# Kernel tuning notes

Measured on AMD Instinct MI355X. Metric: run time of the kernel, lower is better.

## Reference

```python
import jax, jax.numpy as jnp
import numpy as np

N, E, D = 50000, 800000, 128      # nodes, edges, input feature dim
H, HEADS, C = 128, 8, 64          # hidden units, attention heads, classes
HEAD_DIM = H // HEADS
NEG_SLOPE = 0.2


def segment_softmax(scores, seg, num_segments):
    # scores: [E, heads]; softmax over edges sharing the same destination node
    m = jax.ops.segment_max(scores, seg, num_segments=num_segments)
    ex = jnp.exp(scores - m[seg])
    s = jax.ops.segment_sum(ex, seg, num_segments=num_segments)
    return ex / (s[seg] + 1e-9)


def gcn_layer(x, src, dst, W, b):
    # mean-aggregate neighbor features along edges, then linear transform
    agg = jax.ops.segment_sum(x[src], dst, num_segments=N)          # [N, d]
    deg = jax.ops.segment_sum(jnp.ones((E,), x.dtype), dst, num_segments=N)
    agg = agg / jnp.maximum(deg, 1.0)[:, None]
    return agg @ W + b


def gat_layer(x, src, dst, Wg, a_src, a_dst, bg):
    h = (x @ Wg).reshape(N, HEADS, HEAD_DIM)                        # [N, heads, hd]
    e_s = jnp.einsum('nhd,hd->nh', h, a_src)                        # [N, heads]
    e_d = jnp.einsum('nhd,hd->nh', h, a_dst)
    scores = jax.nn.leaky_relu(e_s[src] + e_d[dst], NEG_SLOPE)      # [E, heads]
    alpha = segment_softmax(scores, dst, N)                         # [E, heads]
    msg = h[src] * alpha[:, :, None]                                # [E, heads, hd]
    out = jax.ops.segment_sum(msg, dst, num_segments=N).reshape(N, H)
    return out + bg


def setup_inputs() -> dict:
    key = jax.random.key(0)
    ks = jax.random.split(key, 12)
    s = lambda fan: 1.0 / np.sqrt(fan)
    return {
        'node_features': jax.random.normal(ks[0], (N, D), jnp.float32),
        'edge_index': jax.random.randint(ks[1], (2, E), 0, N, jnp.int32),
        'W1': jax.random.normal(ks[2], (D, H), jnp.float32) * s(D),
        'b1': jnp.zeros((H,), jnp.float32),
        'W2': jax.random.normal(ks[3], (H, H), jnp.float32) * s(H),
        'b2': jnp.zeros((H,), jnp.float32),
        'Wg': jax.random.normal(ks[4], (D, H), jnp.float32) * s(D),
        'bg': jnp.zeros((H,), jnp.float32),
        'a_src': jax.random.normal(ks[5], (HEADS, HEAD_DIM), jnp.float32) * s(HEAD_DIM),
        'a_dst': jax.random.normal(ks[6], (HEADS, HEAD_DIM), jnp.float32) * s(HEAD_DIM),
        'Wcls': jax.random.normal(ks[7], (H, C), jnp.float32) * s(H),
        'bcls': jnp.zeros((C,), jnp.float32),
        'Wl': jax.random.normal(ks[8], (H, 1), jnp.float32) * s(H),
        'bl': jnp.zeros((1,), jnp.float32),
    }


def reference(node_features, edge_index, W1, b1, W2, b2, Wg, bg, a_src, a_dst, Wcls, bcls, Wl, bl):
    src, dst = edge_index[0], edge_index[1]
    x = jax.nn.relu(gcn_layer(node_features, src, dst, W1, b1))
    x = jax.nn.relu(gcn_layer(x, src, dst, W2, b2))
    node_classification_output = jax.nn.softmax(x @ Wcls + bcls, axis=-1)  # [N, C]
    x_gat = jax.nn.relu(gat_layer(node_features, src, dst, Wg, a_src, a_dst, bg))
    link_prediction_output = jax.nn.sigmoid(x_gat @ Wl + bl)               # [N, 1]
    return (node_classification_output, link_prediction_output)
```

## Files before the change

kernel.cpp:

```cpp
#include <hip/hip_runtime.h>
#include <math.h>

#define DIM      128
#define HEADS    8
#define NCLS     64
#define NEG_SLOPE 0.2f
#define NPB32    32
#define NPB64    64
#define APAD     132
#define CAP      48

typedef unsigned int uint32;

__device__ __forceinline__ uint32 pack_bf162(float a, float b) {
    uint32 ua = __float_as_uint(a); ua += 0x7fffu + ((ua >> 16) & 1u);
    uint32 ub = __float_as_uint(b); ub += 0x7fffu + ((ub >> 16) & 1u);
    return (ua >> 16) | (ub & 0xffff0000u);
}
__device__ __forceinline__ float2 unpack_bf162(uint32 u) {
    return make_float2(__uint_as_float(u << 16), __uint_as_float(u & 0xffff0000u));
}

__global__ __launch_bounds__(256, 4)
void proj1_fill(const float* __restrict__ x, const float* __restrict__ W1,
                const float* __restrict__ Wg, const float* __restrict__ a_src,
                const float* __restrict__ a_dst, uint32* __restrict__ zb,
                float* __restrict__ e_s, float* __restrict__ e_d, int N,
                const int* __restrict__ src, const int* __restrict__ dst,
                int* __restrict__ cursor, int* __restrict__ ell, int E,
                int nProj) {
    __shared__ float A[NPB64 * APAD];
    int tid = threadIdx.x;

    if (blockIdx.x >= nProj) {
        int e = (blockIdx.x - nProj) * 256 + tid;
        if (e < E) {
            int d = dst[e];
            int pos = atomicAdd(&cursor[d], 1);
            if (pos < CAP) ell[(size_t)d * CAP + pos] = src[e];
        }
        return;
    }

    int n0 = blockIdx.x * NPB64;
    for (int idx = tid; idx < NPB64 * 32; idx += 256) {
        int nl = idx >> 5, q = idx & 31;
        int n = n0 + nl;
        float4 v = (n < N) ? ((const float4*)x)[(size_t)n * 32 + q]
                           : make_float4(0.f, 0.f, 0.f, 0.f);
        *(float4*)&A[nl * APAD + q * 4] = v;
    }
    __syncthreads();

    int fg = tid & 31, ng = tid >> 5;
    int nb = ng * 8;
    bool isG = fg >= 16;
    const float* W = isG ? (Wg + (size_t)(fg - 16) * 8) : (W1 + (size_t)fg * 8);
    float acc[8][8];
#pragma unroll
    for (int r = 0; r < 8; ++r)
#pragma unroll
        for (int c = 0; c < 8; ++c) acc[r][c] = 0.f;

#pragma unroll 4
    for (int k = 0; k < DIM; ++k) {
        float wv[8];
        *(float4*)&wv[0] = *(const float4*)(W + (size_t)k * DIM);
        *(float4*)&wv[4] = *(const float4*)(W + (size_t)k * DIM + 4);
#pragma unroll
        for (int r = 0; r < 8; ++r) {
            float a = A[(nb + r) * APAD + k];
#pragma unroll
            for (int c = 0; c < 8; ++c) acc[r][c] = fmaf(a, wv[c], acc[r][c]);
        }
    }
#pragma unroll
    for (int r = 0; r < 8; ++r) {
        int n = n0 + nb + r;
        if (n < N) {
            uint32 o[4];
#pragma unroll
            for (int c = 0; c < 4; ++c) o[c] = pack_bf162(acc[r][2 * c], acc[r][2 * c + 1]);
            *(uint4*)(zb + (size_t)n * 128 + fg * 4) = *(uint4*)o;
        }
    }
    if (isG) {
        int head = (fg - 16) >> 1, sub = ((fg - 16) & 1) * 8;
        float as[8], ad[8];
#pragma unroll
        for (int j = 0; j < 8; ++j) {
            as[j] = a_src[head * 16 + sub + j];
            ad[j] = a_dst[head * 16 + sub + j];
        }
#pragma unroll
        for (int r = 0; r < 8; ++r) {
            int n = n0 + nb + r;
            float ps = 0.f, pd = 0.f;
#pragma unroll
            for (int c = 0; c < 8; ++c) {
                ps = fmaf(acc[r][c], as[c], ps);
                pd = fmaf(acc[r][c], ad[c], pd);
            }
            ps += __shfl_xor(ps, 1);
            pd += __shfl_xor(pd, 1);
            if (n < N && !(fg & 1)) {
                e_s[n * HEADS + head] = ps;
                e_d[n * HEADS + head] = pd;
            }
        }
    }
}

__global__ __launch_bounds__(256, 8)
void mega1(const uint32* __restrict__ zb, const int* __restrict__ cursor,
           const int* __restrict__ ell, const float* __restrict__ e_s,
           const float* __restrict__ e_d, const float* __restrict__ b1,
           const float* __restrict__ bg, const float* __restrict__ Wl,
           const float* __restrict__ bl, uint32* __restrict__ x1b,
           float* __restrict__ out_link, int N) {
    int wave = threadIdx.x >> 6, lane = threadIdx.x & 63;
    int n = blockIdx.x * 4 + wave;
    if (n >= N) return;
    int eoff = lane >> 5, q = lane & 31;
    bool isH = q >= 16;
    int head = (max(q, 16) - 16) >> 1;
    float edl = e_d[n * HEADS + head];
    const uint4* zrow = (const uint4*)zb;
    size_t base = (size_t)n * CAP;
    int len = min(cursor[n], CAP);
    float acc[8];
#pragma unroll
    for (int j = 0; j < 8; ++j) acc[j] = 0.f;
    float den = 0.f;
    int it = 0;
    for (; it + 8 <= len; it += 8) {
        int s[4];
#pragma unroll
        for (int k = 0; k < 4; ++k) s[k] = ell[base + it + 2 * k + eoff];
        float es[4]; uint4 u[4];
#pragma unroll
        for (int k = 0; k < 4; ++k) {
            es[k] = e_s[s[k] * HEADS + head];
            u[k]  = zrow[(size_t)s[k] * 32 + q];
        }
#pragma unroll
        for (int k = 0; k < 4; ++k) {
            float sc = es[k] + edl;
            sc = (sc > 0.f) ? sc : NEG_SLOPE * sc;
            float ex = __expf(sc);
            den += ex;
            float w = isH ? ex : 1.f;
            float2 v0 = unpack_bf162(u[k].x), v1 = unpack_bf162(u[k].y);
            float2 v2 = unpack_bf162(u[k].z), v3 = unpack_bf162(u[k].w);
            acc[0] = fmaf(v0.x, w, acc[0]); acc[1] = fmaf(v0.y, w, acc[1]);
            acc[2] = fmaf(v1.x, w, acc[2]); acc[3] = fmaf(v1.y, w, acc[3]);
            acc[4] = fmaf(v2.x, w, acc[4]); acc[5] = fmaf(v2.y, w, acc[5]);
            acc[6] = fmaf(v3.x, w, acc[6]); acc[7] = fmaf(v3.y, w, acc[7]);
        }
    }
    for (; it < len; it += 2) {
        int e = it + eoff;
        bool valid = e < len;
        int s = ell[base + (valid ? e : it)];
        float sc = e_s[s * HEADS + head] + edl;
        sc = (sc > 0.f) ? sc : NEG_SLOPE * sc;
        float ex = __expf(sc);
        uint4 u = zrow[(size_t)s * 32 + q];
        den += valid ? ex : 0.f;
        float w = valid ? (isH ? ex : 1.f) : 0.f;
        float2 v0 = unpack_bf162(u.x), v1 = unpack_bf162(u.y);
        float2 v2 = unpack_bf162(u.z), v3 = unpack_bf162(u.w);
        acc[0] = fmaf(v0.x, w, acc[0]); acc[1] = fmaf(v0.y, w, acc[1]);
        acc[2] = fmaf(v1.x, w, acc[2]); acc[3] = fmaf(v1.y, w, acc[3]);
        acc[4] = fmaf(v2.x, w, acc[4]); acc[5] = fmaf(v2.y, w, acc[5]);
        acc[6] = fmaf(v3.x, w, acc[6]); acc[7] = fmaf(v3.y, w, acc[7]);
    }
#pragma unroll
    for (int j = 0; j < 8; ++j) acc[j] += __shfl_xor(acc[j], 32);
    den += __shfl_xor(den, 32);

    if (!isH && eoff == 0) {
        float inv = 1.f / fmaxf((float)len, 1.f);
        float4 ba = ((const float4*)b1)[2 * q];
        float4 bb = ((const float4*)b1)[2 * q + 1];
        uint4 o;
        o.x = pack_bf162(fmaxf(acc[0] * inv + ba.x, 0.f), fmaxf(acc[1] * inv + ba.y, 0.f));
        o.y = pack_bf162(fmaxf(acc[2] * inv + ba.z, 0.f), fmaxf(acc[3] * inv + ba.w, 0.f));
        o.z = pack_bf162(fmaxf(acc[4] * inv + bb.x, 0.f), fmaxf(acc[5] * inv + bb.y, 0.f));
        o.w = pack_bf162(fmaxf(acc[6] * inv + bb.z, 0.f), fmaxf(acc[7] * inv + bb.w, 0.f));
        ((uint4*)(x1b + (size_t)n * 64))[q] = o;
    }
    float p = 0.f;
    if (isH && eoff == 0) {
        float inva = 1.f / (den + 1e-9f);
        int hq = q - 16;
        float4 ga = ((const float4*)bg)[2 * hq];
        float4 gb = ((const float4*)bg)[2 * hq + 1];
        float4 wa = ((const float4*)Wl)[2 * hq];
        float4 wb = ((const float4*)Wl)[2 * hq + 1];
        p = fmaf(fmaxf(acc[0] * inva + ga.x, 0.f), wa.x, p);
        p = fmaf(fmaxf(acc[1] * inva + ga.y, 0.f), wa.y, p);
        p = fmaf(fmaxf(acc[2] * inva + ga.z, 0.f), wa.z, p);
        p = fmaf(fmaxf(acc[3] * inva + ga.w, 0.f), wa.w, p);
        p = fmaf(fmaxf(acc[4] * inva + gb.x, 0.f), wb.x, p);
        p = fmaf(fmaxf(acc[5] * inva + gb.y, 0.f), wb.y, p);
        p = fmaf(fmaxf(acc[6] * inva + gb.z, 0.f), wb.z, p);
        p = fmaf(fmaxf(acc[7] * inva + gb.w, 0.f), wb.w, p);
    }
#pragma unroll
    for (int off = 1; off < 64; off <<= 1) p += __shfl_xor(p, off);
    if (lane == 0) out_link[n] = 1.f / (1.f + expf(-(p + bl[0])));
}

__global__ __launch_bounds__(256, 4)
void proj2(const uint32* __restrict__ x1b, const float* __restrict__ W2,
           uint32* __restrict__ y2b, int N) {
    __shared__ float A[NPB64 * APAD];
    int n0 = blockIdx.x * NPB64;
    int tid = threadIdx.x;
    for (int idx = tid; idx < NPB64 * 64; idx += 256) {
        int nl = idx >> 6, q = idx & 63;
        int n = n0 + nl;
        float2 v = (n < N) ? unpack_bf162(x1b[(size_t)n * 64 + q]) : make_float2(0.f, 0.f);
        A[nl * APAD + 2 * q]     = v.x;
        A[nl * APAD + 2 * q + 1] = v.y;
    }
    __syncthreads();
    int fg = tid & 15, ng = tid >> 4;
    int nb = ng * 4;
    float acc[4][8];
#pragma unroll
    for (int r = 0; r < 4; ++r)
#pragma unroll
        for (int c = 0; c < 8; ++c) acc[r][c] = 0.f;
    const float4* W4 = (const float4*)W2;
#pragma unroll 4
    for (int k = 0; k < DIM; ++k) {
        float wv[8];
        *(float4*)&wv[0] = W4[k * 32 + fg * 2];
        *(float4*)&wv[4] = W4[k * 32 + fg * 2 + 1];
#pragma unroll
        for (int r = 0; r < 4; ++r) {
            float a = A[(nb + r) * APAD + k];
#pragma unroll
            for (int c = 0; c < 8; ++c) acc[r][c] = fmaf(a, wv[c], acc[r][c]);
        }
    }
#pragma unroll
    for (int r = 0; r < 4; ++r) {
        int n = n0 + nb + r;
        if (n < N) {
            uint32 o[4];
#pragma unroll
            for (int c = 0; c < 4; ++c) o[c] = pack_bf162(acc[r][2 * c], acc[r][2 * c + 1]);
            *(uint4*)(y2b + (size_t)n * 64 + fg * 4) = *(uint4*)o;
        }
    }
}

__global__ __launch_bounds__(256, 8)
void mega2(const uint32* __restrict__ y2b, const int* __restrict__ cursor,
           const int* __restrict__ ell, const float* __restrict__ b2,
           const float* __restrict__ Wcls, const float* __restrict__ bcls,
           float* __restrict__ out_cls, int N) {
    __shared__ float A[NPB32 * APAD];
    int tid = threadIdx.x;
    int wave = tid >> 6, lane = tid & 63;
    int eoff = lane >> 4, q = lane & 15;
    int n0 = blockIdx.x * NPB32;
    const uint4* yrow = (const uint4*)y2b;

    for (int i = 0; i < 8; ++i) {
        int nl = wave * 8 + i;
        int n = n0 + nl;
        int len = (n < N) ? min(cursor[n], CAP) : 0;
        size_t base = (size_t)n * CAP;
        float acc[8];
#pragma unroll
        for (int j = 0; j < 8; ++j) acc[j] = 0.f;
        int it = 0;
        for (; it + 16 <= len; it += 16) {
            int s[4];
#pragma unroll
            for (int k = 0; k < 4; ++k) s[k] = ell[base + it + 4 * k + eoff];
            uint4 u[4];
#pragma unroll
            for (int k = 0; k < 4; ++k) u[k] = yrow[(size_t)s[k] * 16 + q];
#pragma unroll
            for (int k = 0; k < 4; ++k) {
                float2 v0 = unpack_bf162(u[k].x), v1 = unpack_bf162(u[k].y);
                float2 v2 = unpack_bf162(u[k].z), v3 = unpack_bf162(u[k].w);
                acc[0] += v0.x; acc[1] += v0.y; acc[2] += v1.x; acc[3] += v1.y;
                acc[4] += v2.x; acc[5] += v2.y; acc[6] += v3.x; acc[7] += v3.y;
            }
        }
        for (; it + 8 <= len; it += 8) {
            int s[2];
#pragma unroll
            for (int k = 0; k < 2; ++k) s[k] = ell[base + it + 4 * k + eoff];
            uint4 u[2];
#pragma unroll
            for (int k = 0; k < 2; ++k) u[k] = yrow[(size_t)s[k] * 16 + q];
#pragma unroll
            for (int k = 0; k < 2; ++k) {
                float2 v0 = unpack_bf162(u[k].x), v1 = unpack_bf162(u[k].y);
                float2 v2 = unpack_bf162(u[k].z), v3 = unpack_bf162(u[k].w);
                acc[0] += v0.x; acc[1] += v0.y; acc[2] += v1.x; acc[3] += v1.y;
                acc[4] += v2.x; acc[5] += v2.y; acc[6] += v3.x; acc[7] += v3.y;
            }
        }
        for (; it < len; it += 4) {
            int e = it + eoff;
            bool valid = e < len;
            int s = ell[base + (valid ? e : it)];
            uint4 u = yrow[(size_t)s * 16 + q];
            float w = valid ? 1.f : 0.f;
            float2 v0 = unpack_bf162(u.x), v1 = unpack_bf162(u.y);
            float2 v2 = unpack_bf162(u.z), v3 = unpack_bf162(u.w);
            acc[0] = fmaf(v0.x, w, acc[0]); acc[1] = fmaf(v0.y, w, acc[1]);
            acc[2] = fmaf(v1.x, w, acc[2]); acc[3] = fmaf(v1.y, w, acc[3]);
            acc[4] = fmaf(v2.x, w, acc[4]); acc[5] = fmaf(v2.y, w, acc[5]);
            acc[6] = fmaf(v3.x, w, acc[6]); acc[7] = fmaf(v3.y, w, acc[7]);
        }
#pragma unroll
        for (int j = 0; j < 8; ++j) {
            acc[j] += __shfl_xor(acc[j], 16);
            acc[j] += __shfl_xor(acc[j], 32);
        }
        if (eoff == 0) {
            float inv = 1.f / fmaxf((float)len, 1.f);
            float4 ba = ((const float4*)b2)[2 * q];
            float4 bb = ((const float4*)b2)[2 * q + 1];
            float4 xa, xb;
            xa.x = fmaxf(acc[0] * inv + ba.x, 0.f); xa.y = fmaxf(acc[1] * inv + ba.y, 0.f);
            xa.z = fmaxf(acc[2] * inv + ba.z, 0.f); xa.w = fmaxf(acc[3] * inv + ba.w, 0.f);
            xb.x = fmaxf(acc[4] * inv + bb.x, 0.f); xb.y = fmaxf(acc[5] * inv + bb.y, 0.f);
            xb.z = fmaxf(acc[6] * inv + bb.z, 0.f); xb.w = fmaxf(acc[7] * inv + bb.w, 0.f);
            *(float4*)&A[nl * APAD + 8 * q]     = xa;
            *(float4*)&A[nl * APAD + 8 * q + 4] = xb;
        }
    }
    __syncthreads();

    int fg = tid & 15, ng = tid >> 4;
    int nm = ng * 2, c0 = fg * 4;
    float accC[2][4];
#pragma unroll
    for (int r = 0; r < 2; ++r)
#pragma unroll
        for (int c = 0; c < 4; ++c) accC[r][c] = 0.f;
    const float4* Wc4 = (const float4*)Wcls;
#pragma unroll 4
    for (int k = 0; k < DIM; ++k) {
        float a0 = A[nm * APAD + k];
        float a1 = A[(nm + 1) * APAD + k];
        float wv[4];
        *(float4*)&wv[0] = Wc4[k * 16 + fg];
#pragma unroll
        for (int c = 0; c < 4; ++c) {
            accC[0][c] = fmaf(a0, wv[c], accC[0][c]);
            accC[1][c] = fmaf(a1, wv[c], accC[1][c]);
        }
    }
    float4 bv = ((const float4*)bcls)[fg];
    float cb[4] = {bv.x, bv.y, bv.z, bv.w};
#pragma unroll
    for (int r = 0; r < 2; ++r) {
        int n = n0 + nm + r;
        float l[4];
        float m = -1e30f;
#pragma unroll
        for (int c = 0; c < 4; ++c) { l[c] = accC[r][c] + cb[c]; m = fmaxf(m, l[c]); }
        for (int off = 1; off < 16; off <<= 1) m = fmaxf(m, __shfl_xor(m, off));
        float s = 0.f;
#pragma unroll
        for (int c = 0; c < 4; ++c) { l[c] = expf(l[c] - m); s += l[c]; }
        for (int off = 1; off < 16; off <<= 1) s += __shfl_xor(s, off);
        float invs = 1.f / s;
        if (n < N) {
            float4 o = {l[0] * invs, l[1] * invs, l[2] * invs, l[3] * invs};
            *(float4*)(out_cls + (size_t)n * NCLS + c0) = o;
        }
    }
}

extern "C" void kernel_launch(void* const* d_in, const int* in_sizes, int n_in,
                              void* d_out, int out_size, void* d_ws, size_t ws_size,
                              hipStream_t stream) {
    const float* xin   = (const float*)d_in[0];
    const int*   eidx  = (const int*)  d_in[1];
    const float* W1    = (const float*)d_in[2];
    const float* b1    = (const float*)d_in[3];
    const float* W2    = (const float*)d_in[4];
    const float* b2    = (const float*)d_in[5];
    const float* Wg    = (const float*)d_in[6];
    const float* bg    = (const float*)d_in[7];
    const float* a_src = (const float*)d_in[8];
    const float* a_dst = (const float*)d_in[9];
    const float* Wcls  = (const float*)d_in[10];
    const float* bcls  = (const float*)d_in[11];
    const float* Wl    = (const float*)d_in[12];
    const float* bl    = (const float*)d_in[13];

    const int N = in_sizes[0] / DIM;
    const int E = in_sizes[1] / 2;
    const int* src = eidx;
    const int* dst = eidx + E;

    int*    cursor = (int*)d_ws;
    int*    ell    = cursor + ((N + 4) & ~3);
    float*  e_s    = (float*)(ell + (size_t)N * CAP);
    float*  e_d    = e_s + (size_t)N * HEADS;
    uint32* zb     = (uint32*)(e_d + (size_t)N * HEADS);
    uint32* x1b    = zb + (size_t)N * 128;
    uint32* y2b    = zb;

    float* out_cls  = (float*)d_out;
    float* out_link = out_cls + (size_t)N * NCLS;

    int blkE   = (E + 255) / 256;
    int blkN4  = (N + 3) / 4;
    int blkN32 = (N + NPB32 - 1) / NPB32;
    int blkN64 = (N + NPB64 - 1) / NPB64;

    hipMemsetAsync(cursor, 0, (size_t)N * sizeof(int), stream);
    proj1_fill<<<blkN64 + blkE, 256, 0, stream>>>(xin, W1, Wg, a_src, a_dst,
                                                  zb, e_s, e_d, N,
                                                  src, dst, cursor, ell, E, blkN64);

    mega1<<<blkN4, 256, 0, stream>>>(zb, cursor, ell, e_s, e_d,
                                     b1, bg, Wl, bl, x1b, out_link, N);

    proj2<<<blkN64, 256, 0, stream>>>(x1b, W2, y2b, N);

    mega2<<<blkN32, 256, 0, stream>>>(y2b, cursor, ell, b2,
                                      Wcls, bcls, out_cls, N);
}
```

Before: 342.2 us.

## Reorder GCN to aggregate-then-project, fuse dense GEMMs into gather kernels, shrink ELL

```diff
diff --git a/kernel.cpp b/kernel.cpp
--- a/kernel.cpp
+++ b/kernel.cpp
@@ -5,8 +5,8 @@
 #define HEADS    8
 #define NCLS     64
 #define NEG_SLOPE 0.2f
-#define NPB32    32
 #define NPB64    64
+#define NPB16    16
 #define APAD     132
 #define CAP      48
 
@@ -22,13 +22,13 @@
 }
 
 __global__ __launch_bounds__(256, 4)
-void proj1_fill(const float* __restrict__ x, const float* __restrict__ W1,
-                const float* __restrict__ Wg, const float* __restrict__ a_src,
-                const float* __restrict__ a_dst, uint32* __restrict__ zb,
-                float* __restrict__ e_s, float* __restrict__ e_d, int N,
+void proj1_fill(const float* __restrict__ x, const float* __restrict__ Wg,
+                const float* __restrict__ a_src, const float* __restrict__ a_dst,
+                uint32* __restrict__ zb, float* __restrict__ e_s,
+                float* __restrict__ e_d, int N,
                 const int* __restrict__ src, const int* __restrict__ dst,
-                int* __restrict__ cursor, int* __restrict__ ell, int E,
-                int nProj) {
+                int* __restrict__ cursor, unsigned short* __restrict__ ell,
+                int E, int nProj) {
     __shared__ float A[NPB64 * APAD];
     int tid = threadIdx.x;
 
@@ -37,28 +37,40 @@
         if (e < E) {
             int d = dst[e];
             int pos = atomicAdd(&cursor[d], 1);
-            if (pos < CAP) ell[(size_t)d * CAP + pos] = src[e];
+            if (pos < CAP) ell[(size_t)d * CAP + pos] = (unsigned short)src[e];
         }
         return;
     }
 
     int n0 = blockIdx.x * NPB64;
     for (int idx = tid; idx < NPB64 * 32; idx += 256) {
-        int nl = idx >> 5, q = idx & 31;
+        int nl = idx >> 5, qq = idx & 31;
         int n = n0 + nl;
-        float4 v = (n < N) ? ((const float4*)x)[(size_t)n * 32 + q]
+        float4 v = (n < N) ? ((const float4*)x)[(size_t)n * 32 + qq]
                            : make_float4(0.f, 0.f, 0.f, 0.f);
-        *(float4*)&A[nl * APAD + q * 4] = v;
+        *(float4*)&A[nl * APAD + qq * 4] = v;
     }
     __syncthreads();
 
-    int fg = tid & 31, ng = tid >> 5;
-    int nb = ng * 8;
-    bool isG = fg >= 16;
-    const float* W = isG ? (Wg + (size_t)(fg - 16) * 8) : (W1 + (size_t)fg * 8);
-    float acc[8][8];
-#pragma unroll
-    for (int r = 0; r < 8; ++r)
+    for (int idx = tid; idx < NPB64 * 16; idx += 256) {
+        int nl = idx >> 4, u4 = idx & 15;
+        int n = n0 + nl;
+        if (n < N) {
+            float4 va = *(float4*)&A[nl * APAD + u4 * 8];
+            float4 vb = *(float4*)&A[nl * APAD + u4 * 8 + 4];
+            uint4 o;
+            o.x = pack_bf162(va.x, va.y); o.y = pack_bf162(va.z, va.w);
+            o.z = pack_bf162(vb.x, vb.y); o.w = pack_bf162(vb.z, vb.w);
+            *(uint4*)(zb + (size_t)n * 128 + u4 * 4) = o;
+        }
+    }
+
+    int fg = tid & 15, ng = tid >> 4;
+    int nb = ng * 4;
+    const float* W = Wg + (size_t)fg * 8;
+    float acc[4][8];
+#pragma unroll
+    for (int r = 0; r < 4; ++r)
 #pragma unroll
         for (int c = 0; c < 8; ++c) acc[r][c] = 0.f;
 
@@ -68,210 +80,192 @@
         *(float4*)&wv[0] = *(const float4*)(W + (size_t)k * DIM);
         *(float4*)&wv[4] = *(const float4*)(W + (size_t)k * DIM + 4);
 #pragma unroll
-        for (int r = 0; r < 8; ++r) {
+        for (int r = 0; r < 4; ++r) {
             float a = A[(nb + r) * APAD + k];
 #pragma unroll
             for (int c = 0; c < 8; ++c) acc[r][c] = fmaf(a, wv[c], acc[r][c]);
         }
     }
 #pragma unroll
-    for (int r = 0; r < 8; ++r) {
+    for (int r = 0; r < 4; ++r) {
         int n = n0 + nb + r;
         if (n < N) {
             uint32 o[4];
 #pragma unroll
             for (int c = 0; c < 4; ++c) o[c] = pack_bf162(acc[r][2 * c], acc[r][2 * c + 1]);
-            *(uint4*)(zb + (size_t)n * 128 + fg * 4) = *(uint4*)o;
-        }
-    }
-    if (isG) {
-        int head = (fg - 16) >> 1, sub = ((fg - 16) & 1) * 8;
-        float as[8], ad[8];
-#pragma unroll
-        for (int j = 0; j < 8; ++j) {
-            as[j] = a_src[head * 16 + sub + j];
-            ad[j] = a_dst[head * 16 + sub + j];
-        }
-#pragma unroll
-        for (int r = 0; r < 8; ++r) {
-            int n = n0 + nb + r;
-            float ps = 0.f, pd = 0.f;
-#pragma unroll
-            for (int c = 0; c < 8; ++c) {
-                ps = fmaf(acc[r][c], as[c], ps);
-                pd = fmaf(acc[r][c], ad[c], pd);
-            }
-            ps += __shfl_xor(ps, 1);
-            pd += __shfl_xor(pd, 1);
-            if (n < N && !(fg & 1)) {
-                e_s[n * HEADS + head] = ps;
-                e_d[n * HEADS + head] = pd;
-            }
+            *(uint4*)(zb + (size_t)n * 128 + 64 + fg * 4) = *(uint4*)o;
+        }
+    }
+    int head = fg >> 1, sub = (fg & 1) * 8;
+    float as[8], ad[8];
+#pragma unroll
+    for (int j = 0; j < 8; ++j) {
+        as[j] = a_src[head * 16 + sub + j];
+        ad[j] = a_dst[head * 16 + sub + j];
+    }
+#pragma unroll
+    for (int r = 0; r < 4; ++r) {
+        int n = n0 + nb + r;
+        float ps = 0.f, pd = 0.f;
+#pragma unroll
+        for (int c = 0; c < 8; ++c) {
+            ps = fmaf(acc[r][c], as[c], ps);
+            pd = fmaf(acc[r][c], ad[c], pd);
+        }
+        ps += __shfl_xor(ps, 1);
+        pd += __shfl_xor(pd, 1);
+        if (n < N && !(fg & 1)) {
+            e_s[n * HEADS + head] = ps;
+            e_d[n * HEADS + head] = pd;
         }
     }
 }
 
 __global__ __launch_bounds__(256, 8)
 void mega1(const uint32* __restrict__ zb, const int* __restrict__ cursor,
-           const int* __restrict__ ell, const float* __restrict__ e_s,
-           const float* __restrict__ e_d, const float* __restrict__ b1,
-           const float* __restrict__ bg, const float* __restrict__ Wl,
-           const float* __restrict__ bl, uint32* __restrict__ x1b,
-           float* __restrict__ out_link, int N) {
-    int wave = threadIdx.x >> 6, lane = threadIdx.x & 63;
-    int n = blockIdx.x * 4 + wave;
-    if (n >= N) return;
+           const unsigned short* __restrict__ ell, const float* __restrict__ e_s,
+           const float* __restrict__ e_d, const float* __restrict__ W1,
+           const float* __restrict__ b1, const float* __restrict__ bg,
+           const float* __restrict__ Wl, const float* __restrict__ bl,
+           uint32* __restrict__ x1b, float* __restrict__ out_link, int N) {
+    __shared__ float A[NPB16 * APAD];
+    int tid = threadIdx.x;
+    int wave = tid >> 6, lane = tid & 63;
     int eoff = lane >> 5, q = lane & 31;
     bool isH = q >= 16;
     int head = (max(q, 16) - 16) >> 1;
-    float edl = e_d[n * HEADS + head];
+    int n0 = blockIdx.x * NPB16;
     const uint4* zrow = (const uint4*)zb;
-    size_t base = (size_t)n * CAP;
-    int len = min(cursor[n], CAP);
-    float acc[8];
-#pragma unroll
-    for (int j = 0; j < 8; ++j) acc[j] = 0.f;
-    float den = 0.f;
-    int it = 0;
-    for (; it + 8 <= len; it += 8) {
-        int s[4];
-#pragma unroll
-        for (int k = 0; k < 4; ++k) s[k] = ell[base + it + 2 * k + eoff];
-        float es[4]; uint4 u[4];
-#pragma unroll
-        for (int k = 0; k < 4; ++k) {
-            es[k] = e_s[s[k] * HEADS + head];
-            u[k]  = zrow[(size_t)s[k] * 32 + q];
-        }
-#pragma unroll
-        for (int k = 0; k < 4; ++k) {
-            float sc = es[k] + edl;
+
+    for (int i = 0; i < 4; ++i) {
+        int nl = wave * 4 + i;
+        int n = n0 + nl;
+        int len = (n < N) ? min(cursor[n], CAP) : 0;
+        size_t base = (size_t)n * CAP;
+        float edl = (n < N) ? e_d[n * HEADS + head] : 0.f;
+        float acc[8];
+#pragma unroll
+        for (int j = 0; j < 8; ++j) acc[j] = 0.f;
+        float den = 0.f;
+        int it = 0;
+        for (; it + 8 <= len; it += 8) {
+            int s[4];
+#pragma unroll
+            for (int k = 0; k < 4; ++k) s[k] = ell[base + it + 2 * k + eoff];
+            float es[4]; uint4 u[4];
+#pragma unroll
+            for (int k = 0; k < 4; ++k) {
+                es[k] = e_s[s[k] * HEADS + head];
+                u[k]  = zrow[(size_t)s[k] * 32 + q];
+            }
+#pragma unroll
+            for (int k = 0; k < 4; ++k) {
+                float sc = es[k] + edl;
+                sc = (sc > 0.f) ? sc : NEG_SLOPE * sc;
+                float ex = __expf(sc);
+                den += ex;
+                float w = isH ? ex : 1.f;
+                float2 v0 = unpack_bf162(u[k].x), v1 = unpack_bf162(u[k].y);
+                float2 v2 = unpack_bf162(u[k].z), v3 = unpack_bf162(u[k].w);
+                acc[0] = fmaf(v0.x, w, acc[0]); acc[1] = fmaf(v0.y, w, acc[1]);
+                acc[2] = fmaf(v1.x, w, acc[2]); acc[3] = fmaf(v1.y, w, acc[3]);
+                acc[4] = fmaf(v2.x, w, acc[4]); acc[5] = fmaf(v2.y, w, acc[5]);
+                acc[6] = fmaf(v3.x, w, acc[6]); acc[7] = fmaf(v3.y, w, acc[7]);
+            }
+        }
+        for (; it < len; it += 2) {
+            int e = it + eoff;
+            bool valid = e < len;
+            int s = ell[base + (valid ? e : it)];
+            float sc = e_s[s * HEADS + head] + edl;
             sc = (sc > 0.f) ? sc : NEG_SLOPE * sc;
             float ex = __expf(sc);
-            den += ex;
-            float w = isH ? ex : 1.f;
-            float2 v0 = unpack_bf162(u[k].x), v1 = unpack_bf162(u[k].y);
-            float2 v2 = unpack_bf162(u[k].z), v3 = unpack_bf162(u[k].w);
+            uint4 u = zrow[(size_t)s * 32 + q];
+            den += valid ? ex : 0.f;
+            float w = valid ? (isH ? ex : 1.f) : 0.f;
+            float2 v0 = unpack_bf162(u.x), v1 = unpack_bf162(u.y);
+            float2 v2 = unpack_bf162(u.z), v3 = unpack_bf162(u.w);
             acc[0] = fmaf(v0.x, w, acc[0]); acc[1] = fmaf(v0.y, w, acc[1]);
             acc[2] = fmaf(v1.x, w, acc[2]); acc[3] = fmaf(v1.y, w, acc[3]);
             acc[4] = fmaf(v2.x, w, acc[4]); acc[5] = fmaf(v2.y, w, acc[5]);
             acc[6] = fmaf(v3.x, w, acc[6]); acc[7] = fmaf(v3.y, w, acc[7]);
         }
-    }
-    for (; it < len; it += 2) {
-        int e = it + eoff;
-        bool valid = e < len;
-        int s = ell[base + (valid ? e : it)];
-        float sc = e_s[s * HEADS + head] + edl;
-        sc = (sc > 0.f) ? sc : NEG_SLOPE * sc;
-        float ex = __expf(sc);
-        uint4 u = zrow[(size_t)s * 32 + q];
-        den += valid ? ex : 0.f;
-        float w = valid ? (isH ? ex : 1.f) : 0.f;
-        float2 v0 = unpack_bf162(u.x), v1 = unpack_bf162(u.y);
-        float2 v2 = unpack_bf162(u.z), v3 = unpack_bf162(u.w);
-        acc[0] = fmaf(v0.x, w, acc[0]); acc[1] = fmaf(v0.y, w, acc[1]);
-        acc[2] = fmaf(v1.x, w, acc[2]); acc[3] = fmaf(v1.y, w, acc[3]);
-        acc[4] = fmaf(v2.x, w, acc[4]); acc[5] = fmaf(v2.y, w, acc[5]);
-        acc[6] = fmaf(v3.x, w, acc[6]); acc[7] = fmaf(v3.y, w, acc[7]);
-    }
-#pragma unroll
-    for (int j = 0; j < 8; ++j) acc[j] += __shfl_xor(acc[j], 32);
-    den += __shfl_xor(den, 32);
-
-    if (!isH && eoff == 0) {
-        float inv = 1.f / fmaxf((float)len, 1.f);
-        float4 ba = ((const float4*)b1)[2 * q];
-        float4 bb = ((const float4*)b1)[2 * q + 1];
-        uint4 o;
-        o.x = pack_bf162(fmaxf(acc[0] * inv + ba.x, 0.f), fmaxf(acc[1] * inv + ba.y, 0.f));
-        o.y = pack_bf162(fmaxf(acc[2] * inv + ba.z, 0.f), fmaxf(acc[3] * inv + ba.w, 0.f));
-        o.z = pack_bf162(fmaxf(acc[4] * inv + bb.x, 0.f), fmaxf(acc[5] * inv + bb.y, 0.f));
-        o.w = pack_bf162(fmaxf(acc[6] * inv + bb.z, 0.f), fmaxf(acc[7] * inv + bb.w, 0.f));
-        ((uint4*)(x1b + (size_t)n * 64))[q] = o;
-    }
-    float p = 0.f;
-    if (isH && eoff == 0) {
-        float inva = 1.f / (den + 1e-9f);
-        int hq = q - 16;
-        float4 ga = ((const float4*)bg)[2 * hq];
-        float4 gb = ((const float4*)bg)[2 * hq + 1];
-        float4 wa = ((const float4*)Wl)[2 * hq];
-        float4 wb = ((const float4*)Wl)[2 * hq + 1];
-        p = fmaf(fmaxf(acc[0] * inva + ga.x, 0.f), wa.x, p);
-        p = fmaf(fmaxf(acc[1] * inva + ga.y, 0.f), wa.y, p);
-        p = fmaf(fmaxf(acc[2] * inva + ga.z, 0.f), wa.z, p);
-        p = fmaf(fmaxf(acc[3] * inva + ga.w, 0.f), wa.w, p);
-        p = fmaf(fmaxf(acc[4] * inva + gb.x, 0.f), wb.x, p);
-        p = fmaf(fmaxf(acc[5] * inva + gb.y, 0.f), wb.y, p);
-        p = fmaf(fmaxf(acc[6] * inva + gb.z, 0.f), wb.z, p);
-        p = fmaf(fmaxf(acc[7] * inva + gb.w, 0.f), wb.w, p);
-    }
-#pragma unroll
-    for (int off = 1; off < 64; off <<= 1) p += __shfl_xor(p, off);
-    if (lane == 0) out_link[n] = 1.f / (1.f + expf(-(p + bl[0])));
-}
-
-__global__ __launch_bounds__(256, 4)
-void proj2(const uint32* __restrict__ x1b, const float* __restrict__ W2,
-           uint32* __restrict__ y2b, int N) {
-    __shared__ float A[NPB64 * APAD];
-    int n0 = blockIdx.x * NPB64;
-    int tid = threadIdx.x;
-    for (int idx = tid; idx < NPB64 * 64; idx += 256) {
-        int nl = idx >> 6, q = idx & 63;
-        int n = n0 + nl;
-        float2 v = (n < N) ? unpack_bf162(x1b[(size_t)n * 64 + q]) : make_float2(0.f, 0.f);
-        A[nl * APAD + 2 * q]     = v.x;
-        A[nl * APAD + 2 * q + 1] = v.y;
+#pragma unroll
+        for (int j = 0; j < 8; ++j) acc[j] += __shfl_xor(acc[j], 32);
+        den += __shfl_xor(den, 32);
+
+        if (!isH && eoff == 0) {
+            float inv = 1.f / fmaxf((float)len, 1.f);
+            *(float4*)&A[nl * APAD + q * 8] =
+                make_float4(acc[0] * inv, acc[1] * inv, acc[2] * inv, acc[3] * inv);
+            *(float4*)&A[nl * APAD + q * 8 + 4] =
+                make_float4(acc[4] * inv, acc[5] * inv, acc[6] * inv, acc[7] * inv);
+        }
+        float p = 0.f;
+        if (isH && eoff == 0) {
+            float inva = 1.f / (den + 1e-9f);
+            int hq = q - 16;
+            float4 ga = ((const float4*)bg)[2 * hq];
+            float4 gb = ((const float4*)bg)[2 * hq + 1];
+            float4 wa = ((const float4*)Wl)[2 * hq];
+            float4 wb = ((const float4*)Wl)[2 * hq + 1];
+            p = fmaf(fmaxf(acc[0] * inva + ga.x, 0.f), wa.x, p);
+            p = fmaf(fmaxf(acc[1] * inva + ga.y, 0.f), wa.y, p);
+            p = fmaf(fmaxf(acc[2] * inva + ga.z, 0.f), wa.z, p);
+            p = fmaf(fmaxf(acc[3] * inva + ga.w, 0.f), wa.w, p);
+            p = fmaf(fmaxf(acc[4] * inva + gb.x, 0.f), wb.x, p);
+            p = fmaf(fmaxf(acc[5] * inva + gb.y, 0.f), wb.y, p);
+            p = fmaf(fmaxf(acc[6] * inva + gb.z, 0.f), wb.z, p);
+            p = fmaf(fmaxf(acc[7] * inva + gb.w, 0.f), wb.w, p);
+        }
+#pragma unroll
+        for (int off = 1; off < 64; off <<= 1) p += __shfl_xor(p, off);
+        if (lane == 0 && n < N) out_link[n] = 1.f / (1.f + expf(-(p + bl[0])));
     }
     __syncthreads();
+
     int fg = tid & 15, ng = tid >> 4;
-    int nb = ng * 4;
-    float acc[4][8];
-#pragma unroll
-    for (int r = 0; r < 4; ++r)
-#pragma unroll
-        for (int c = 0; c < 8; ++c) acc[r][c] = 0.f;
-    const float4* W4 = (const float4*)W2;
+    float acc2[8];
+#pragma unroll
+    for (int c = 0; c < 8; ++c) acc2[c] = 0.f;
+    const float* W = W1 + (size_t)fg * 8;
 #pragma unroll 4
     for (int k = 0; k < DIM; ++k) {
+        float a = A[ng * APAD + k];
         float wv[8];
-        *(float4*)&wv[0] = W4[k * 32 + fg * 2];
-        *(float4*)&wv[4] = W4[k * 32 + fg * 2 + 1];
-#pragma unroll
-        for (int r = 0; r < 4; ++r) {
-            float a = A[(nb + r) * APAD + k];
-#pragma unroll
-            for (int c = 0; c < 8; ++c) acc[r][c] = fmaf(a, wv[c], acc[r][c]);
-        }
-    }
-#pragma unroll
-    for (int r = 0; r < 4; ++r) {
-        int n = n0 + nb + r;
-        if (n < N) {
-            uint32 o[4];
-#pragma unroll
-            for (int c = 0; c < 4; ++c) o[c] = pack_bf162(acc[r][2 * c], acc[r][2 * c + 1]);
-            *(uint4*)(y2b + (size_t)n * 64 + fg * 4) = *(uint4*)o;
-        }
+        *(float4*)&wv[0] = *(const float4*)(W + (size_t)k * DIM);
+        *(float4*)&wv[4] = *(const float4*)(W + (size_t)k * DIM + 4);
+#pragma unroll
+        for (int c = 0; c < 8; ++c) acc2[c] = fmaf(a, wv[c], acc2[c]);
+    }
+    int n = n0 + ng;
+    if (n < N) {
+        float bv[8];
+        *(float4*)&bv[0] = ((const float4*)b1)[fg * 2];
+        *(float4*)&bv[4] = ((const float4*)b1)[fg * 2 + 1];
+        uint32 o[4];
+#pragma unroll
+        for (int c = 0; c < 4; ++c)
+            o[c] = pack_bf162(fmaxf(acc2[2 * c] + bv[2 * c], 0.f),
+                              fmaxf(acc2[2 * c + 1] + bv[2 * c + 1], 0.f));
+        *(uint4*)(x1b + (size_t)n * 64 + fg * 4) = *(uint4*)o;
     }
 }
 
 __global__ __launch_bounds__(256, 8)
-void mega2(const uint32* __restrict__ y2b, const int* __restrict__ cursor,
-           const int* __restrict__ ell, const float* __restrict__ b2,
-           const float* __restrict__ Wcls, const float* __restrict__ bcls,
-           float* __restrict__ out_cls, int N) {
-    __shared__ float A[NPB32 * APAD];
+void mega2(const uint32* __restrict__ x1b, const int* __restrict__ cursor,
+           const unsigned short* __restrict__ ell, const float* __restrict__ W2,
+           const float* __restrict__ b2, const float* __restrict__ Wcls,
+           const float* __restrict__ bcls, float* __restrict__ out_cls, int N) {
+    __shared__ float A[NPB16 * APAD];
     int tid = threadIdx.x;
     int wave = tid >> 6, lane = tid & 63;
     int eoff = lane >> 4, q = lane & 15;
-    int n0 = blockIdx.x * NPB32;
-    const uint4* yrow = (const uint4*)y2b;
-
-    for (int i = 0; i < 8; ++i) {
-        int nl = wave * 8 + i;
+    int n0 = blockIdx.x * NPB16;
+    const uint4* yrow = (const uint4*)x1b;
+
+    for (int i = 0; i < 4; ++i) {
+        int nl = wave * 4 + i;
         int n = n0 + nl;
         int len = (n < N) ? min(cursor[n], CAP) : 0;
         size_t base = (size_t)n * CAP;
@@ -329,58 +323,67 @@
         }
         if (eoff == 0) {
             float inv = 1.f / fmaxf((float)len, 1.f);
-            float4 ba = ((const float4*)b2)[2 * q];
-            float4 bb = ((const float4*)b2)[2 * q + 1];
-            float4 xa, xb;
-            xa.x = fmaxf(acc[0] * inv + ba.x, 0.f); xa.y = fmaxf(acc[1] * inv + ba.y, 0.f);
-            xa.z = fmaxf(acc[2] * inv + ba.z, 0.f); xa.w = fmaxf(acc[3] * inv + ba.w, 0.f);
-            xb.x = fmaxf(acc[4] * inv + bb.x, 0.f); xb.y = fmaxf(acc[5] * inv + bb.y, 0.f);
-            xb.z = fmaxf(acc[6] * inv + bb.z, 0.f); xb.w = fmaxf(acc[7] * inv + bb.w, 0.f);
-            *(float4*)&A[nl * APAD + 8 * q]     = xa;
-            *(float4*)&A[nl * APAD + 8 * q + 4] = xb;
+            *(float4*)&A[nl * APAD + 8 * q] =
+                make_float4(acc[0] * inv, acc[1] * inv, acc[2] * inv, acc[3] * inv);
+            *(float4*)&A[nl * APAD + 8 * q + 4] =
+                make_float4(acc[4] * inv, acc[5] * inv, acc[6] * inv, acc[7] * inv);
         }
     }
     __syncthreads();
 
     int fg = tid & 15, ng = tid >> 4;
-    int nm = ng * 2, c0 = fg * 4;
-    float accC[2][4];
-#pragma unroll
-    for (int r = 0; r < 2; ++r)
-#pragma unroll
-        for (int c = 0; c < 4; ++c) accC[r][c] = 0.f;
-    const float4* Wc4 = (const float4*)Wcls;
+    float acc2[8];
+#pragma unroll
+    for (int c = 0; c < 8; ++c) acc2[c] = 0.f;
+    const float* W = W2 + (size_t)fg * 8;
 #pragma unroll 4
     for (int k = 0; k < DIM; ++k) {
-        float a0 = A[nm * APAD + k];
-        float a1 = A[(nm + 1) * APAD + k];
+        float a = A[ng * APAD + k];
+        float wv[8];
+        *(float4*)&wv[0] = *(const float4*)(W + (size_t)k * DIM);
+        *(float4*)&wv[4] = *(const float4*)(W + (size_t)k * DIM + 4);
+#pragma unroll
+        for (int c = 0; c < 8; ++c) acc2[c] = fmaf(a, wv[c], acc2[c]);
+    }
+    float bv[8];
+    *(float4*)&bv[0] = ((const float4*)b2)[fg * 2];
+    *(float4*)&bv[4] = ((const float4*)b2)[fg * 2 + 1];
+    __syncthreads();
+    *(float4*)&A[ng * APAD + fg * 8] =
+        make_float4(fmaxf(acc2[0] + bv[0], 0.f), fmaxf(acc2[1] + bv[1], 0.f),
+                    fmaxf(acc2[2] + bv[2], 0.f), fmaxf(acc2[3] + bv[3], 0.f));
+    *(float4*)&A[ng * APAD + fg * 8 + 4] =
+        make_float4(fmaxf(acc2[4] + bv[4], 0.f), fmaxf(acc2[5] + bv[5], 0.f),
+                    fmaxf(acc2[6] + bv[6], 0.f), fmaxf(acc2[7] + bv[7], 0.f));
+    __syncthreads();
+
+    int c0 = fg * 4;
+    float accC[4];
+#pragma unroll
+    for (int c = 0; c < 4; ++c) accC[c] = 0.f;
+#pragma unroll 4
+    for (int k = 0; k < DIM; ++k) {
+        float a = A[ng * APAD + k];
         float wv[4];
-        *(float4*)&wv[0] = Wc4[k * 16 + fg];
-#pragma unroll
-        for (int c = 0; c < 4; ++c) {
-            accC[0][c] = fmaf(a0, wv[c], accC[0][c]);
-            accC[1][c] = fmaf(a1, wv[c], accC[1][c]);
-        }
-    }
-    float4 bv = ((const float4*)bcls)[fg];
-    float cb[4] = {bv.x, bv.y, bv.z, bv.w};
-#pragma unroll
-    for (int r = 0; r < 2; ++r) {
-        int n = n0 + nm + r;
-        float l[4];
-        float m = -1e30f;
-#pragma unroll
-        for (int c = 0; c < 4; ++c) { l[c] = accC[r][c] + cb[c]; m = fmaxf(m, l[c]); }
-        for (int off = 1; off < 16; off <<= 1) m = fmaxf(m, __shfl_xor(m, off));
-        float s = 0.f;
-#pragma unroll
-        for (int c = 0; c < 4; ++c) { l[c] = expf(l[c] - m); s += l[c]; }
-        for (int off = 1; off < 16; off <<= 1) s += __shfl_xor(s, off);
+        *(float4*)&wv[0] = *(const float4*)(Wcls + (size_t)k * NCLS + c0);
+#pragma unroll
+        for (int c = 0; c < 4; ++c) accC[c] = fmaf(a, wv[c], accC[c]);
+    }
+    float4 bcv = ((const float4*)bcls)[fg];
+    float l[4];
+    l[0] = accC[0] + bcv.x; l[1] = accC[1] + bcv.y;
+    l[2] = accC[2] + bcv.z; l[3] = accC[3] + bcv.w;
+    float m = fmaxf(fmaxf(l[0], l[1]), fmaxf(l[2], l[3]));
+    for (int off = 1; off < 16; off <<= 1) m = fmaxf(m, __shfl_xor(m, off));
+    float s = 0.f;
+#pragma unroll
+    for (int c = 0; c < 4; ++c) { l[c] = expf(l[c] - m); s += l[c]; }
+    for (int off = 1; off < 16; off <<= 1) s += __shfl_xor(s, off);
+    int n = n0 + ng;
+    if (n < N) {
         float invs = 1.f / s;
-        if (n < N) {
-            float4 o = {l[0] * invs, l[1] * invs, l[2] * invs, l[3] * invs};
-            *(float4*)(out_cls + (size_t)n * NCLS + c0) = o;
-        }
+        float4 o = {l[0] * invs, l[1] * invs, l[2] * invs, l[3] * invs};
+        *(float4*)(out_cls + (size_t)n * NCLS + c0) = o;
     }
 }
 
@@ -407,32 +410,35 @@
     const int* src = eidx;
     const int* dst = eidx + E;
 
-    int*    cursor = (int*)d_ws;
-    int*    ell    = cursor + ((N + 4) & ~3);
-    float*  e_s    = (float*)(ell + (size_t)N * CAP);
-    float*  e_d    = e_s + (size_t)N * HEADS;
-    uint32* zb     = (uint32*)(e_d + (size_t)N * HEADS);
-    uint32* x1b    = zb + (size_t)N * 128;
-    uint32* y2b    = zb;
+    char* ws = (char*)d_ws;
+    size_t off = 0;
+    int* cursor = (int*)(ws + off);
+    off = (off + (size_t)N * sizeof(int) + 15) & ~(size_t)15;
+    unsigned short* ell = (unsigned short*)(ws + off);
+    off = (off + (size_t)N * CAP * sizeof(unsigned short) + 15) & ~(size_t)15;
+    float* e_s = (float*)(ws + off);
+    off = (off + (size_t)N * HEADS * sizeof(float) + 15) & ~(size_t)15;
+    float* e_d = (float*)(ws + off);
+    off = (off + (size_t)N * HEADS * sizeof(float) + 15) & ~(size_t)15;
+    uint32* zb = (uint32*)(ws + off);
+    off = (off + (size_t)N * 128 * sizeof(uint32) + 15) & ~(size_t)15;
+    uint32* x1b = (uint32*)(ws + off);
 
     float* out_cls  = (float*)d_out;
     float* out_link = out_cls + (size_t)N * NCLS;
 
     int blkE   = (E + 255) / 256;
-    int blkN4  = (N + 3) / 4;
-    int blkN32 = (N + NPB32 - 1) / NPB32;
     int blkN64 = (N + NPB64 - 1) / NPB64;
+    int blkN16 = (N + NPB16 - 1) / NPB16;
 
     hipMemsetAsync(cursor, 0, (size_t)N * sizeof(int), stream);
-    proj1_fill<<<blkN64 + blkE, 256, 0, stream>>>(xin, W1, Wg, a_src, a_dst,
+    proj1_fill<<<blkN64 + blkE, 256, 0, stream>>>(xin, Wg, a_src, a_dst,
                                                   zb, e_s, e_d, N,
                                                   src, dst, cursor, ell, E, blkN64);
 
-    mega1<<<blkN4, 256, 0, stream>>>(zb, cursor, ell, e_s, e_d,
-                                     b1, bg, Wl, bl, x1b, out_link, N);
-
-    proj2<<<blkN64, 256, 0, stream>>>(x1b, W2, y2b, N);
-
-    mega2<<<blkN32, 256, 0, stream>>>(y2b, cursor, ell, b2,
+    mega1<<<blkN16, 256, 0, stream>>>(zb, cursor, ell, e_s, e_d,
+                                      W1, b1, bg, Wl, bl, x1b, out_link, N);
+
+    mega2<<<blkN16, 256, 0, stream>>>(x1b, cursor, ell, W2, b2,
                                       Wcls, bcls, out_cls, N);
 }
```

New measurement: 497.9 us. +45.5%, slower.

## Aggregate raw features before W1, fuse W1/W2 GEMMs, shrink ELL to u16

Applied to the files above, without the earlier changes.

```diff
diff --git a/kernel.cpp b/kernel.cpp
--- a/kernel.cpp
+++ b/kernel.cpp
@@ -22,13 +22,13 @@
 }
 
 __global__ __launch_bounds__(256, 4)
-void proj1_fill(const float* __restrict__ x, const float* __restrict__ W1,
-                const float* __restrict__ Wg, const float* __restrict__ a_src,
-                const float* __restrict__ a_dst, uint32* __restrict__ zb,
-                float* __restrict__ e_s, float* __restrict__ e_d, int N,
+void proj1_fill(const float* __restrict__ x, const float* __restrict__ Wg,
+                const float* __restrict__ a_src, const float* __restrict__ a_dst,
+                uint32* __restrict__ zb, float* __restrict__ e_s,
+                float* __restrict__ e_d, int N,
                 const int* __restrict__ src, const int* __restrict__ dst,
-                int* __restrict__ cursor, int* __restrict__ ell, int E,
-                int nProj) {
+                int* __restrict__ cursor, unsigned short* __restrict__ ell,
+                int E, int nProj) {
     __shared__ float A[NPB64 * APAD];
     int tid = threadIdx.x;
 
@@ -37,28 +37,40 @@
         if (e < E) {
             int d = dst[e];
             int pos = atomicAdd(&cursor[d], 1);
-            if (pos < CAP) ell[(size_t)d * CAP + pos] = src[e];
+            if (pos < CAP) ell[(size_t)d * CAP + pos] = (unsigned short)src[e];
         }
         return;
     }
 
     int n0 = blockIdx.x * NPB64;
     for (int idx = tid; idx < NPB64 * 32; idx += 256) {
-        int nl = idx >> 5, q = idx & 31;
+        int nl = idx >> 5, qq = idx & 31;
         int n = n0 + nl;
-        float4 v = (n < N) ? ((const float4*)x)[(size_t)n * 32 + q]
+        float4 v = (n < N) ? ((const float4*)x)[(size_t)n * 32 + qq]
                            : make_float4(0.f, 0.f, 0.f, 0.f);
-        *(float4*)&A[nl * APAD + q * 4] = v;
+        *(float4*)&A[nl * APAD + qq * 4] = v;
     }
     __syncthreads();
 
-    int fg = tid & 31, ng = tid >> 5;
-    int nb = ng * 8;
-    bool isG = fg >= 16;
-    const float* W = isG ? (Wg + (size_t)(fg - 16) * 8) : (W1 + (size_t)fg * 8);
-    float acc[8][8];
-#pragma unroll
-    for (int r = 0; r < 8; ++r)
+    for (int idx = tid; idx < NPB64 * 16; idx += 256) {
+        int nl = idx >> 4, u4 = idx & 15;
+        int n = n0 + nl;
+        if (n < N) {
+            float4 va = *(float4*)&A[nl * APAD + u4 * 8];
+            float4 vb = *(float4*)&A[nl * APAD + u4 * 8 + 4];
+            uint4 o;
+            o.x = pack_bf162(va.x, va.y); o.y = pack_bf162(va.z, va.w);
+            o.z = pack_bf162(vb.x, vb.y); o.w = pack_bf162(vb.z, vb.w);
+            *(uint4*)(zb + (size_t)n * 128 + u4 * 4) = o;
+        }
+    }
+
+    int fg = tid & 15, ng = tid >> 4;
+    int nb = ng * 4;
+    const float* W = Wg + (size_t)fg * 8;
+    float acc[4][8];
+#pragma unroll
+    for (int r = 0; r < 4; ++r)
 #pragma unroll
         for (int c = 0; c < 8; ++c) acc[r][c] = 0.f;
 
@@ -68,56 +80,53 @@
         *(float4*)&wv[0] = *(const float4*)(W + (size_t)k * DIM);
         *(float4*)&wv[4] = *(const float4*)(W + (size_t)k * DIM + 4);
 #pragma unroll
-        for (int r = 0; r < 8; ++r) {
+        for (int r = 0; r < 4; ++r) {
             float a = A[(nb + r) * APAD + k];
 #pragma unroll
             for (int c = 0; c < 8; ++c) acc[r][c] = fmaf(a, wv[c], acc[r][c]);
         }
     }
 #pragma unroll
-    for (int r = 0; r < 8; ++r) {
+    for (int r = 0; r < 4; ++r) {
         int n = n0 + nb + r;
         if (n < N) {
             uint32 o[4];
 #pragma unroll
             for (int c = 0; c < 4; ++c) o[c] = pack_bf162(acc[r][2 * c], acc[r][2 * c + 1]);
-            *(uint4*)(zb + (size_t)n * 128 + fg * 4) = *(uint4*)o;
-        }
-    }
-    if (isG) {
-        int head = (fg - 16) >> 1, sub = ((fg - 16) & 1) * 8;
-        float as[8], ad[8];
-#pragma unroll
-        for (int j = 0; j < 8; ++j) {
-            as[j] = a_src[head * 16 + sub + j];
-            ad[j] = a_dst[head * 16 + sub + j];
-        }
-#pragma unroll
-        for (int r = 0; r < 8; ++r) {
-            int n = n0 + nb + r;
-            float ps = 0.f, pd = 0.f;
-#pragma unroll
-            for (int c = 0; c < 8; ++c) {
-                ps = fmaf(acc[r][c], as[c], ps);
-                pd = fmaf(acc[r][c], ad[c], pd);
-            }
-            ps += __shfl_xor(ps, 1);
-            pd += __shfl_xor(pd, 1);
-            if (n < N && !(fg & 1)) {
-                e_s[n * HEADS + head] = ps;
-                e_d[n * HEADS + head] = pd;
-            }
+            *(uint4*)(zb + (size_t)n * 128 + 64 + fg * 4) = *(uint4*)o;
+        }
+    }
+    int head = fg >> 1, sub = (fg & 1) * 8;
+    float as[8], ad[8];
+#pragma unroll
+    for (int j = 0; j < 8; ++j) {
+        as[j] = a_src[head * 16 + sub + j];
+        ad[j] = a_dst[head * 16 + sub + j];
+    }
+#pragma unroll
+    for (int r = 0; r < 4; ++r) {
+        int n = n0 + nb + r;
+        float ps = 0.f, pd = 0.f;
+#pragma unroll
+        for (int c = 0; c < 8; ++c) {
+            ps = fmaf(acc[r][c], as[c], ps);
+            pd = fmaf(acc[r][c], ad[c], pd);
+        }
+        ps += __shfl_xor(ps, 1);
+        pd += __shfl_xor(pd, 1);
+        if (n < N && !(fg & 1)) {
+            e_s[n * HEADS + head] = ps;
+            e_d[n * HEADS + head] = pd;
         }
     }
 }
 
 __global__ __launch_bounds__(256, 8)
 void mega1(const uint32* __restrict__ zb, const int* __restrict__ cursor,
-           const int* __restrict__ ell, const float* __restrict__ e_s,
-           const float* __restrict__ e_d, const float* __restrict__ b1,
-           const float* __restrict__ bg, const float* __restrict__ Wl,
-           const float* __restrict__ bl, uint32* __restrict__ x1b,
-           float* __restrict__ out_link, int N) {
+           const unsigned short* __restrict__ ell, const float* __restrict__ e_s,
+           const float* __restrict__ e_d, const float* __restrict__ bg,
+           const float* __restrict__ Wl, const float* __restrict__ bl,
+           uint32* __restrict__ mxb, float* __restrict__ out_link, int N) {
     int wave = threadIdx.x >> 6, lane = threadIdx.x & 63;
     int n = blockIdx.x * 4 + wave;
     if (n >= N) return;
@@ -181,14 +190,12 @@
 
     if (!isH && eoff == 0) {
         float inv = 1.f / fmaxf((float)len, 1.f);
-        float4 ba = ((const float4*)b1)[2 * q];
-        float4 bb = ((const float4*)b1)[2 * q + 1];
         uint4 o;
-        o.x = pack_bf162(fmaxf(acc[0] * inv + ba.x, 0.f), fmaxf(acc[1] * inv + ba.y, 0.f));
-        o.y = pack_bf162(fmaxf(acc[2] * inv + ba.z, 0.f), fmaxf(acc[3] * inv + ba.w, 0.f));
-        o.z = pack_bf162(fmaxf(acc[4] * inv + bb.x, 0.f), fmaxf(acc[5] * inv + bb.y, 0.f));
-        o.w = pack_bf162(fmaxf(acc[6] * inv + bb.z, 0.f), fmaxf(acc[7] * inv + bb.w, 0.f));
-        ((uint4*)(x1b + (size_t)n * 64))[q] = o;
+        o.x = pack_bf162(acc[0] * inv, acc[1] * inv);
+        o.y = pack_bf162(acc[2] * inv, acc[3] * inv);
+        o.z = pack_bf162(acc[4] * inv, acc[5] * inv);
+        o.w = pack_bf162(acc[6] * inv, acc[7] * inv);
+        ((uint4*)(mxb + (size_t)n * 64))[q] = o;
     }
     float p = 0.f;
     if (isH && eoff == 0) {
@@ -213,19 +220,21 @@
 }
 
 __global__ __launch_bounds__(256, 4)
-void proj2(const uint32* __restrict__ x1b, const float* __restrict__ W2,
-           uint32* __restrict__ y2b, int N) {
+void proj12(const uint32* __restrict__ mxb, const float* __restrict__ W1,
+            const float* __restrict__ b1, const float* __restrict__ W2,
+            uint32* __restrict__ y2b, int N) {
     __shared__ float A[NPB64 * APAD];
     int n0 = blockIdx.x * NPB64;
     int tid = threadIdx.x;
     for (int idx = tid; idx < NPB64 * 64; idx += 256) {
         int nl = idx >> 6, q = idx & 63;
         int n = n0 + nl;
-        float2 v = (n < N) ? unpack_bf162(x1b[(size_t)n * 64 + q]) : make_float2(0.f, 0.f);
+        float2 v = (n < N) ? unpack_bf162(mxb[(size_t)n * 64 + q]) : make_float2(0.f, 0.f);
         A[nl * APAD + 2 * q]     = v.x;
         A[nl * APAD + 2 * q + 1] = v.y;
     }
     __syncthreads();
+
     int fg = tid & 15, ng = tid >> 4;
     int nb = ng * 4;
     float acc[4][8];
@@ -233,12 +242,44 @@
     for (int r = 0; r < 4; ++r)
 #pragma unroll
         for (int c = 0; c < 8; ++c) acc[r][c] = 0.f;
-    const float4* W4 = (const float4*)W2;
+    const float* Wa = W1 + (size_t)fg * 8;
 #pragma unroll 4
     for (int k = 0; k < DIM; ++k) {
         float wv[8];
-        *(float4*)&wv[0] = W4[k * 32 + fg * 2];
-        *(float4*)&wv[4] = W4[k * 32 + fg * 2 + 1];
+        *(float4*)&wv[0] = *(const float4*)(Wa + (size_t)k * DIM);
+        *(float4*)&wv[4] = *(const float4*)(Wa + (size_t)k * DIM + 4);
+#pragma unroll
+        for (int r = 0; r < 4; ++r) {
+            float a = A[(nb + r) * APAD + k];
+#pragma unroll
+            for (int c = 0; c < 8; ++c) acc[r][c] = fmaf(a, wv[c], acc[r][c]);
+        }
+    }
+    float bv[8];
+    *(float4*)&bv[0] = ((const float4*)b1)[fg * 2];
+    *(float4*)&bv[4] = ((const float4*)b1)[fg * 2 + 1];
+    __syncthreads();
+#pragma unroll
+    for (int r = 0; r < 4; ++r) {
+        *(float4*)&A[(nb + r) * APAD + fg * 8] =
+            make_float4(fmaxf(acc[r][0] + bv[0], 0.f), fmaxf(acc[r][1] + bv[1], 0.f),
+                        fmaxf(acc[r][2] + bv[2], 0.f), fmaxf(acc[r][3] + bv[3], 0.f));
+        *(float4*)&A[(nb + r) * APAD + fg * 8 + 4] =
+            make_float4(fmaxf(acc[r][4] + bv[4], 0.f), fmaxf(acc[r][5] + bv[5], 0.f),
+                        fmaxf(acc[r][6] + bv[6], 0.f), fmaxf(acc[r][7] + bv[7], 0.f));
+    }
+    __syncthreads();
+
+#pragma unroll
+    for (int r = 0; r < 4; ++r)
+#pragma unroll
+        for (int c = 0; c < 8; ++c) acc[r][c] = 0.f;
+    const float* Wb = W2 + (size_t)fg * 8;
+#pragma unroll 4
+    for (int k = 0; k < DIM; ++k) {
+        float wv[8];
+        *(float4*)&wv[0] = *(const float4*)(Wb + (size_t)k * DIM);
+        *(float4*)&wv[4] = *(const float4*)(Wb + (size_t)k * DIM + 4);
 #pragma unroll
         for (int r = 0; r < 4; ++r) {
             float a = A[(nb + r) * APAD + k];
@@ -260,7 +301,7 @@
 
 __global__ __launch_bounds__(256, 8)
 void mega2(const uint32* __restrict__ y2b, const int* __restrict__ cursor,
-           const int* __restrict__ ell, const float* __restrict__ b2,
+           const unsigned short* __restrict__ ell, const float* __restrict__ b2,
            const float* __restrict__ Wcls, const float* __restrict__ bcls,
            float* __restrict__ out_cls, int N) {
     __shared__ float A[NPB32 * APAD];
@@ -407,13 +448,20 @@
     const int* src = eidx;
     const int* dst = eidx + E;
 
-    int*    cursor = (int*)d_ws;
-    int*    ell    = cursor + ((N + 4) & ~3);
-    float*  e_s    = (float*)(ell + (size_t)N * CAP);
-    float*  e_d    = e_s + (size_t)N * HEADS;
-    uint32* zb     = (uint32*)(e_d + (size_t)N * HEADS);
-    uint32* x1b    = zb + (size_t)N * 128;
-    uint32* y2b    = zb;
+    char* ws = (char*)d_ws;
+    size_t off = 0;
+    int* cursor = (int*)(ws + off);
+    off = (off + (size_t)N * sizeof(int) + 15) & ~(size_t)15;
+    unsigned short* ell = (unsigned short*)(ws + off);
+    off = (off + (size_t)N * CAP * sizeof(unsigned short) + 15) & ~(size_t)15;
+    float* e_s = (float*)(ws + off);
+    off = (off + (size_t)N * HEADS * sizeof(float) + 15) & ~(size_t)15;
+    float* e_d = (float*)(ws + off);
+    off = (off + (size_t)N * HEADS * sizeof(float) + 15) & ~(size_t)15;
+    uint32* zb = (uint32*)(ws + off);
+    off = (off + (size_t)N * 128 * sizeof(uint32) + 15) & ~(size_t)15;
+    uint32* mxb = (uint32*)(ws + off);
+    uint32* y2b = zb;
 
     float* out_cls  = (float*)d_out;
     float* out_link = out_cls + (size_t)N * NCLS;
@@ -424,14 +472,14 @@
     int blkN64 = (N + NPB64 - 1) / NPB64;
 
     hipMemsetAsync(cursor, 0, (size_t)N * sizeof(int), stream);
-    proj1_fill<<<blkN64 + blkE, 256, 0, stream>>>(xin, W1, Wg, a_src, a_dst,
+    proj1_fill<<<blkN64 + blkE, 256, 0, stream>>>(xin, Wg, a_src, a_dst,
                                                   zb, e_s, e_d, N,
                                                   src, dst, cursor, ell, E, blkN64);
 
     mega1<<<blkN4, 256, 0, stream>>>(zb, cursor, ell, e_s, e_d,
-                                     b1, bg, Wl, bl, x1b, out_link, N);
-
-    proj2<<<blkN64, 256, 0, stream>>>(x1b, W2, y2b, N);
+                                     bg, Wl, bl, mxb, out_link, N);
+
+    proj12<<<blkN64, 256, 0, stream>>>(mxb, W1, b1, W2, y2b, N);
 
     mega2<<<blkN32, 256, 0, stream>>>(y2b, cursor, ell, b2,
                                       Wcls, bcls, out_cls, N);
```

After: 372.1 us. +8.7%, slower.
